# Optimization experiments

Hardware: AMD Instinct MI355X
Metric: run time of the kernel (lower is better)

The kernel has to match this reference:

```python
import jax, jax.numpy as jnp
import numpy as np

BN_EPS = 1e-5

def batchnorm2d(x, gamma, beta):
    # x: [B, H, *, *]; normalize over (B, dim2, dim3) per channel H (training-mode batch stats)
    mean = jnp.mean(x, axis=(0, 2, 3), keepdims=True)
    var = jnp.var(x, axis=(0, 2, 3), keepdims=True)
    xhat = (x - mean) * jax.lax.rsqrt(var + BN_EPS)
    return xhat * gamma[None, :, None, None] + beta[None, :, None, None]

def setup_inputs() -> dict:
    key = jax.random.key(0)
    ks = jax.random.split(key, 8)
    B, N, C = 64, 196, 768
    H = 12
    hd = C // H  # 64
    patch = 196  # img_size**2, must equal N
    x = jax.random.normal(ks[0], (B, N, C), dtype=jnp.float32)
    W_qv = jax.random.normal(ks[1], (C, 2 * C), dtype=jnp.float32) * (1.0 / np.sqrt(C))
    k_ext = jax.random.normal(ks[2], (patch, hd), dtype=jnp.float32)  # torch init: ones; randomized for testing
    attn_bias = jax.random.normal(ks[3], (1, patch), dtype=jnp.float32) * 0.02
    bn_gamma = jnp.ones((H,), dtype=jnp.float32) + 0.1 * jax.random.normal(ks[4], (H,), dtype=jnp.float32)
    bn_beta = 0.1 * jax.random.normal(ks[5], (H,), dtype=jnp.float32)
    W_proj = jax.random.normal(ks[6], (C, C), dtype=jnp.float32) * (1.0 / np.sqrt(C))
    b_proj = jnp.zeros((C,), dtype=jnp.float32)
    return {"x": x, "W_qv": W_qv, "k_ext": k_ext, "attn_bias": attn_bias,
            "bn_gamma": bn_gamma, "bn_beta": bn_beta, "W_proj": W_proj, "b_proj": b_proj}

def reference(x, W_qv, k_ext, attn_bias, bn_gamma, bn_beta, W_proj, b_proj):
    B, N, C = x.shape
    H = bn_gamma.shape[0]
    hd = C // H
    scale = hd ** -0.5
    # qv projection: [B,N,2C] -> q,v each [B,H,N,hd]
    qv = (x @ W_qv).reshape(B, N, 2, H, hd).transpose(2, 0, 3, 1, 4)
    q, v = qv[0], qv[1]
    # scores against fixed k_ext: [B,H,N,patch]
    attn = jnp.einsum('bhnd,pd->bhnp', q, k_ext)
    attn = (batchnorm2d(attn, bn_gamma, bn_beta) + attn_bias) * scale
    attn = jax.nn.softmax(attn, axis=-1)
    v = batchnorm2d(v, bn_gamma, bn_beta)
    out = jnp.einsum('bhnp,bhpd->bhnd', attn, v)  # patch == N
    out = out.transpose(0, 2, 1, 3).reshape(B, N, C)
    return out @ W_proj + b_proj
```

## Files before the change

kernel.cpp:

```cpp
#include <hip/hip_runtime.h>
#include <hip/hip_bf16.h>

typedef __bf16 b16;
typedef __bf16 b16x8 __attribute__((ext_vector_type(8)));
typedef float  f32x4 __attribute__((ext_vector_type(4)));

#define B_   64
#define N_   196
#define C_   768
#define H_   12
#define HD_  64
#define TOK  (B_*N_)
#define SCALE 0.125f

__device__ __forceinline__ void gl_lds16(const void* g, void* l){
  __builtin_amdgcn_global_load_lds((const __attribute__((address_space(1))) void*)g,
                                   (__attribute__((address_space(3))) void*)l, 16, 0, 0);
}

__global__ __launch_bounds__(256) void k_transpose_cvt(const float* __restrict__ in,
                                                       b16* __restrict__ out, int R, int C){
  __shared__ b16 tile[32][33];
  int tx = threadIdx.x, ty = threadIdx.y;
  int bx = blockIdx.x, by = blockIdx.y;
  int c = bx*32 + tx;
  #pragma unroll
  for (int i = 0; i < 32; i += 8){
    int r = by*32 + ty + i;
    tile[ty+i][tx] = (b16)in[(long)r*C + c];
  }
  __syncthreads();
  int rr = by*32 + tx;
  #pragma unroll
  for (int i = 0; i < 32; i += 8){
    int cc = bx*32 + ty + i;
    out[(long)cc*R + rr] = tile[tx][ty+i];
  }
}

__global__ __launch_bounds__(256) void k_cvt(const float* __restrict__ in, b16* __restrict__ out){
  long i = ((long)blockIdx.x*256 + threadIdx.x)*8;
  const float4* s = (const float4*)(in + i);
  float4 f0 = s[0], f1 = s[1];
  b16x8 v; v[0]=(b16)f0.x; v[1]=(b16)f0.y; v[2]=(b16)f0.z; v[3]=(b16)f0.w;
           v[4]=(b16)f1.x; v[5]=(b16)f1.y; v[6]=(b16)f1.z; v[7]=(b16)f1.w;
  *(b16x8*)(out + i) = v;
}

__global__ __launch_bounds__(256) void k_kprep(const float* __restrict__ k_ext,
                                               float* __restrict__ Kmat, float* __restrict__ ksum){
  __shared__ float ks[N_][HD_];
  int tid = threadIdx.x, blk = blockIdx.x;
  for (int i = tid; i < N_*HD_; i += 256) ks[i/HD_][i%HD_] = k_ext[i];
  __syncthreads();
  int i = tid >> 2;
  int j0 = blk*16 + (tid & 3)*4;
  float a0=0.f, a1=0.f, a2=0.f, a3=0.f;
  for (int p = 0; p < N_; ++p){
    float ki = ks[p][i];
    float4 kv = *(const float4*)&ks[p][j0];
    a0 += ki*kv.x; a1 += ki*kv.y; a2 += ki*kv.z; a3 += ki*kv.w;
  }
  Kmat[i*64+j0+0]=a0; Kmat[i*64+j0+1]=a1; Kmat[i*64+j0+2]=a2; Kmat[i*64+j0+3]=a3;
  if (blk == 0 && tid < 64){
    float s = 0.f;
    for (int p = 0; p < N_; ++p) s += ks[p][tid];
    ksum[tid] = s;
  }
}

template<int MODE>
__global__ __launch_bounds__(256) void k_gemm(const b16* __restrict__ A,
                                              const b16* __restrict__ BT,
                                              b16* __restrict__ qout, b16* __restrict__ vout,
                                              float* __restrict__ fout, const float* __restrict__ bias,
                                              const float* __restrict__ ksum, float* __restrict__ stats){
  const int NT  = (MODE == 0) ? 12 : 6;
  const int NWG = 98*NT;
  int orig = blockIdx.x;
  int q8 = NWG >> 3, r8 = NWG & 7;
  int xcd = orig & 7, loc = orig >> 3;
  int bid = (xcd < r8 ? xcd*(q8+1) : r8*(q8+1) + (xcd-r8)*q8) + loc;
  int rt = bid / NT, ct = bid % NT;
  int brow = rt*128, bcol = ct*128;

  __shared__ b16 sm[2][2][128*32];
  int tid = threadIdx.x, lane = tid & 63, w = tid >> 6;
  int wr = w >> 1, wc = w & 1;

  int rsub = w*16 + (lane>>2);
  int gsrc = (lane & 3) ^ ((lane >> 3) & 3);
  const b16* gA = A  + (long)(brow + rsub)*768 + gsrc*8;
  const b16* gB = BT + (long)(bcol + rsub)*768 + gsrc*8;
  b16* lA0 = &sm[0][0][w*16*32];
  b16* lB0 = &sm[0][1][w*16*32];
  b16* lA1 = &sm[1][0][w*16*32];
  b16* lB1 = &sm[1][1][w*16*32];

#define STAGE(la, lb, kt) do{ \
    gl_lds16(gA + (kt)*32,            (la));        \
    gl_lds16(gA + (kt)*32 + 64*768,   (la) + 64*32);\
    gl_lds16(gB + (kt)*32,            (lb));        \
    gl_lds16(gB + (kt)*32 + 64*768,   (lb) + 64*32);\
  } while(0)

#define COMPUTE(cur) do{ \
    const char* smA = (const char*)sm[cur][0]; \
    const char* smB = (const char*)sm[cur][1]; \
    b16x8 af[4], bf[4]; \
    _Pragma("unroll") \
    for (int m = 0; m < 4; ++m){ \
      int row = wr*64 + m*16 + (lane & 15); \
      af[m] = *(const b16x8*)(smA + row*64 + (((lane>>4) ^ ((row>>1)&3))<<4)); \
    } \
    _Pragma("unroll") \
    for (int n = 0; n < 4; ++n){ \
      int row = wc*64 + n*16 + (lane & 15); \
      bf[n] = *(const b16x8*)(smB + row*64 + (((lane>>4) ^ ((row>>1)&3))<<4)); \
    } \
    _Pragma("unroll") \
    for (int m = 0; m < 4; ++m) \
      _Pragma("unroll") \
      for (int n = 0; n < 4; ++n) \
        acc[m][n] = __builtin_amdgcn_mfma_f32_16x16x32_bf16(af[m], bf[n], acc[m][n], 0, 0, 0); \
  } while(0)

  f32x4 acc[4][4];
  #pragma unroll
  for (int m = 0; m < 4; ++m)
    #pragma unroll
    for (int n = 0; n < 4; ++n) acc[m][n] = (f32x4){0.f,0.f,0.f,0.f};

  STAGE(lA0, lB0, 0);
  STAGE(lA1, lB1, 1);

  #pragma unroll 1
  for (int kt = 0; kt < 23; ++kt){
    int cur = kt & 1;
    asm volatile("s_waitcnt vmcnt(4)" ::: "memory");
    __builtin_amdgcn_s_barrier();
    asm volatile("" ::: "memory");
    COMPUTE(cur);
    asm volatile("" ::: "memory");
    __builtin_amdgcn_s_barrier();
    asm volatile("" ::: "memory");
    if (kt < 22){
      if (cur == 0) STAGE(lA0, lB0, kt+2);
      else          STAGE(lA1, lB1, kt+2);
    }
  }
  asm volatile("s_waitcnt vmcnt(0)" ::: "memory");
  __builtin_amdgcn_s_barrier();
  asm volatile("" ::: "memory");
  COMPUTE(1);
#undef COMPUTE
#undef STAGE

  if constexpr (MODE == 0){
    #pragma unroll
    for (int m = 0; m < 4; ++m){
      #pragma unroll
      for (int n = 0; n < 4; ++n){
        int col = bcol + wc*64 + n*16 + (lane & 15);
        int two = (col >= 768) ? 1 : 0;
        int hc = col - two*768;
        int hh = hc >> 6, d = hc & 63;
        b16* dst = two ? vout : qout;
        #pragma unroll
        for (int j = 0; j < 4; ++j){
          int r2 = brow + wr*64 + m*16 + ((lane>>4)<<2) + j;
          int bq = r2 / 196;
          int nn = r2 - bq*196;
          dst[((bq*12 + hh)*196 + nn)*64 + d] = (b16)acc[m][n][j];
        }
      }
    }
    {
      bool isV = (bcol >= 768);
      float a_acc = 0.f, b_acc = 0.f;
      #pragma unroll
      for (int n = 0; n < 4; ++n){
        int d = n*16 + (lane & 15);
        float s = 0.f, s2 = 0.f;
        #pragma unroll
        for (int m = 0; m < 4; ++m)
          #pragma unroll
          for (int j = 0; j < 4; ++j){
            float v = acc[m][n][j];
            s += v; s2 += v*v;
          }
        if (isV){ a_acc += s; b_acc += s2; }
        else      a_acc += s * ksum[d];
      }
      #pragma unroll
      for (int off = 1; off < 64; off <<= 1){
        a_acc += __shfl_xor(a_acc, off, 64);
        b_acc += __shfl_xor(b_acc, off, 64);
      }
      if (lane == 0){
        if (isV){
          int hv = 2*(ct - 6) + wc;
          atomicAdd(&stats[24 + hv], a_acc);
          atomicAdd(&stats[36 + hv], b_acc);
        } else {
          int hq = 2*ct + wc;
          atomicAdd(&stats[hq], a_acc);
        }
      }
    }
  } else {
    #pragma unroll
    for (int m = 0; m < 4; ++m){
      #pragma unroll
      for (int n = 0; n < 4; ++n){
        int col = bcol + wc*64 + n*16 + (lane & 15);
        float bv = bias[col];
        #pragma unroll
        for (int j = 0; j < 4; ++j){
          int r2 = brow + wr*64 + m*16 + ((lane>>4)<<2) + j;
          fout[(long)r2*768 + col] = acc[m][n][j] + bv;
        }
      }
    }
  }
}

__global__ __launch_bounds__(256) void k_gram(const b16* __restrict__ qb, float* __restrict__ G){
  __shared__ b16 qT[64*232];
  int tid = threadIdx.x, lane = tid & 63, w = tid >> 6;
  int h = blockIdx.x % 12, bg = blockIdx.x / 12;
  f32x4 acc[4];
  #pragma unroll
  for (int n = 0; n < 4; ++n) acc[n] = (f32x4){0.f,0.f,0.f,0.f};
  #pragma unroll 1
  for (int r = 0; r < 2; ++r){
    int b = bg*2 + r;
    const b16* src = qb + ((long)(b*12 + h))*196*64;
    int d = lane;
    for (int p0 = w*8; p0 < 224; p0 += 32){
      b16x8 w8;
      #pragma unroll
      for (int j = 0; j < 8; ++j){
        int p = p0 + j;
        w8[j] = (p < 196) ? src[p*64 + d] : (b16)0.f;
      }
      *(b16x8*)(qT + d*232 + p0) = w8;
    }
    __syncthreads();
    #pragma unroll
    for (int ks = 0; ks < 7; ++ks){
      int t0 = ks*32;
      b16x8 af = *(const b16x8*)(qT + (16*w + (lane&15))*232 + t0 + ((lane>>4)<<3));
      #pragma unroll
      for (int n = 0; n < 4; ++n){
        b16x8 bf = *(const b16x8*)(qT + (16*n + (lane&15))*232 + t0 + ((lane>>4)<<3));
        acc[n] = __builtin_amdgcn_mfma_f32_16x16x32_bf16(af, bf, acc[n], 0, 0, 0);
      }
    }
    __syncthreads();
  }
  float* Gh = G + h*4096;
  #pragma unroll
  for (int n = 0; n < 4; ++n)
    #pragma unroll
    for (int j = 0; j < 4; ++j){
      int i  = 16*w + ((lane>>4)<<2) + j;
      int jj = 16*n + (lane&15);
      atomicAdd(&Gh[i*64 + jj], acc[n][j]);
    }
}

__global__ __launch_bounds__(256) void k_sfin(const float* __restrict__ G, const float* __restrict__ Kmat,
                                              const float* __restrict__ stats, const float* __restrict__ gamma,
                                              const float* __restrict__ beta, float* __restrict__ coef){
  int h = blockIdx.x, tid = threadIdx.x;
  const float* Gh = G + h*4096;
  float s = 0.f;
  #pragma unroll
  for (int k = 0; k < 16; ++k) s += Gh[tid + k*256]*Kmat[tid + k*256];
  #pragma unroll
  for (int off = 1; off < 64; off <<= 1) s += __shfl_xor(s, off, 64);
  __shared__ float red[4];
  if ((tid & 63) == 0) red[tid>>6] = s;
  __syncthreads();
  if (tid == 0){
    float S2 = red[0]+red[1]+red[2]+red[3];
    const float cntS = 2458624.f, cntV = 802816.f;
    float S1 = stats[h], VS = stats[24+h], VS2 = stats[36+h];
    float ms = S1/cntS;
    float vars = S2/cntS - ms*ms;
    float alpha = gamma[h]*SCALE*rsqrtf(vars + 1e-5f);
    float mv = VS/cntV;
    float varv = VS2/cntV - mv*mv;
    float a = gamma[h]*rsqrtf(varv + 1e-5f);
    coef[h*4+0] = alpha;
    coef[h*4+1] = a;
    coef[h*4+2] = beta[h] - a*mv;
  }
}

__global__ __launch_bounds__(256, 2) void k_attn(const b16* __restrict__ qb, const b16* __restrict__ vb,
                                                 const float* __restrict__ k_ext,
                                                 const float* __restrict__ attn_bias,
                                                 const float* __restrict__ coef,
                                                 b16* __restrict__ Ob){
  __shared__ b16 ksh[196*64];
  __shared__ b16 vsh[64*216];
  __shared__ b16 psh[4][16*200];
  __shared__ float bsh[196];

  int tid = threadIdx.x, lane = tid & 63, wid = tid >> 6;
  int bh = blockIdx.x;
  int h = bh % 12, b = bh / 12;
  const b16* qt = qb + (long)bh*N_*64;
  const b16* vt = vb + (long)bh*N_*64;
  float alpha = coef[h*4+0], av = coef[h*4+1], cv = coef[h*4+2];

  for (int c = tid; c < 196*8; c += 256){
    int p = c >> 3, g = c & 7;
    const float4* src = (const float4*)(k_ext + p*64 + g*8);
    float4 f0 = src[0], f1 = src[1];
    b16x8 v; v[0]=(b16)f0.x; v[1]=(b16)f0.y; v[2]=(b16)f0.z; v[3]=(b16)f0.w;
             v[4]=(b16)f1.x; v[5]=(b16)f1.y; v[6]=(b16)f1.z; v[7]=(b16)f1.w;
    *(b16x8*)((char*)ksh + p*128 + ((g ^ (p&7))<<4)) = v;
  }
  for (int p = tid; p < 196; p += 256) bsh[p] = attn_bias[p]*SCALE;
  {
    int d = tid & 63;
    for (int p0 = (tid>>6)*8; p0 < 196; p0 += 32){
      b16x8 w;
      #pragma unroll
      for (int j = 0; j < 8; ++j){
        int p = p0 + j;
        w[j] = (p < 196) ? vt[p*64 + d] : (b16)0.f;
      }
      *(b16x8*)((char*)vsh + d*432 + p0*2) = w;
    }
  }
  __syncthreads();

  for (int rt = wid; rt < 13; rt += 4){
    int n0 = rt*16;
    int qrow = n0 + (lane & 15); if (qrow > 195) qrow = 195;
    b16x8 a0 = *(const b16x8*)((const char*)qt + qrow*128 +      ((lane>>4)<<4));
    b16x8 a1 = *(const b16x8*)((const char*)qt + qrow*128 + 64 + ((lane>>4)<<4));

    f32x4 sc[13];
    #pragma unroll
    for (int ct = 0; ct < 13; ++ct){
      int p = ct*16 + (lane & 15); int pc = p > 195 ? 195 : p;
      b16x8 b0 = *(const b16x8*)((const char*)ksh + pc*128 + ((( (lane>>4))   ^ (pc&7))<<4));
      b16x8 b1 = *(const b16x8*)((const char*)ksh + pc*128 + (((4+(lane>>4))  ^ (pc&7))<<4));
      f32x4 z = {0.f,0.f,0.f,0.f};
      z = __builtin_amdgcn_mfma_f32_16x16x32_bf16(a0, b0, z, 0, 0, 0);
      z = __builtin_amdgcn_mfma_f32_16x16x32_bf16(a1, b1, z, 0, 0, 0);
      sc[ct] = z;
    }
    int pcol = lane & 15;
    float mx[4] = {-1e30f,-1e30f,-1e30f,-1e30f};
    #pragma unroll
    for (int ct = 0; ct < 13; ++ct){
      int p = ct*16 + pcol;
      bool valid = (p < 196);
      float badd = valid ? bsh[p < 196 ? p : 0] : 0.f;
      #pragma unroll
      for (int j = 0; j < 4; ++j){
        float lv = valid ? (sc[ct][j]*alpha + badd) : -1e30f;
        sc[ct][j] = lv;
        mx[j] = fmaxf(mx[j], lv);
      }
    }
    #pragma unroll
    for (int off = 1; off < 16; off <<= 1)
      #pragma unroll
      for (int j = 0; j < 4; ++j) mx[j] = fmaxf(mx[j], __shfl_xor(mx[j], off, 64));
    float sm[4] = {0.f,0.f,0.f,0.f};
    #pragma unroll
    for (int ct = 0; ct < 13; ++ct)
      #pragma unroll
      for (int j = 0; j < 4; ++j){
        float e = __expf(sc[ct][j] - mx[j]);
        sc[ct][j] = e; sm[j] += e;
      }
    #pragma unroll
    for (int off = 1; off < 16; off <<= 1)
      #pragma unroll
      for (int j = 0; j < 4; ++j) sm[j] += __shfl_xor(sm[j], off, 64);
    float rs[4];
    #pragma unroll
    for (int j = 0; j < 4; ++j) rs[j] = 1.f/sm[j];

    b16* pw = psh[wid];
    #pragma unroll
    for (int ct = 0; ct < 12; ++ct){
      int p = ct*16 + pcol;
      #pragma unroll
      for (int j = 0; j < 4; ++j){
        int r = ((lane>>4)<<2) + j;
        pw[r*200 + p] = (b16)(sc[ct][j]*rs[j]);
      }
    }
    float pt12[4];
    #pragma unroll
    for (int j = 0; j < 4; ++j) pt12[j] = sc[12][j]*rs[j];

    __asm__ volatile("s_waitcnt lgkmcnt(0)" ::: "memory");
    __builtin_amdgcn_sched_barrier(0);

    f32x4 o[4];
    #pragma unroll
    for (int dt = 0; dt < 4; ++dt) o[dt] = (f32x4){0.f,0.f,0.f,0.f};
    #pragma unroll
    for (int pt = 0; pt < 6; ++pt){
      b16x8 pa = *(const b16x8*)((const char*)pw + (lane&15)*400 + pt*64 + ((lane>>4)<<4));
      #pragma unroll
      for (int dt = 0; dt < 4; ++dt){
        b16x8 vf = *(const b16x8*)((const char*)vsh + (dt*16 + (lane&15))*432 + pt*64 + ((lane>>4)<<4));
        o[dt] = __builtin_amdgcn_mfma_f32_16x16x32_bf16(pa, vf, o[dt], 0, 0, 0);
      }
    }
    #pragma unroll
    for (int e = 0; e < 4; ++e){
      float pe[4];
      #pragma unroll
      for (int j = 0; j < 4; ++j) pe[j] = __shfl(pt12[j], (lane & 48) + e, 64);
      #pragma unroll
      for (int dt = 0; dt < 4; ++dt){
        b16 vv = *((const b16*)((const char*)vsh + (dt*16 + (lane&15))*432 + (192+e)*2));
        float vvf = (float)vv;
        #pragma unroll
        for (int j = 0; j < 4; ++j) o[dt][j] += pe[j]*vvf;
      }
    }
    #pragma unroll
    for (int dt = 0; dt < 4; ++dt)
      #pragma unroll
      for (int j = 0; j < 4; ++j){
        int n = n0 + ((lane>>4)<<2) + j;
        if (n < 196){
          long idx = ((long)(b*196 + n))*768 + h*64 + dt*16 + (lane&15);
          Ob[idx] = (b16)(av*o[dt][j] + cv);
        }
      }
  }
}

extern "C" void kernel_launch(void* const* d_in, const int* in_sizes, int n_in,
                              void* d_out, int out_size, void* d_ws, size_t ws_size,
                              hipStream_t stream){
  const float* x         = (const float*)d_in[0];
  const float* W_qv      = (const float*)d_in[1];
  const float* k_ext     = (const float*)d_in[2];
  const float* attn_bias = (const float*)d_in[3];
  const float* bn_gamma  = (const float*)d_in[4];
  const float* bn_beta   = (const float*)d_in[5];
  const float* W_proj    = (const float*)d_in[6];
  const float* b_proj    = (const float*)d_in[7];
  float* out = (float*)d_out;

  char* ws = (char*)d_ws;
  const long SZ = 19267584;
  b16*   q_buf   = (b16*)(ws);
  b16*   v_buf   = (b16*)(ws + SZ);
  b16*   O_buf   = (b16*)(ws + 2*SZ);
  b16*   x_bf16  = (b16*)(ws + 2*SZ);
  b16*   W_qvT   = (b16*)(ws + 3*SZ);
  b16*   W_projT = (b16*)(ws + 3*SZ + 2359296);
  float* Kmat    = (float*)(ws + 3*SZ + 3538944);
  float* ksum    = Kmat + 4096;
  float* stats   = ksum + 64;
  float* coef    = stats + 48;
  float* Ggram   = coef + 48;

  hipMemsetAsync(stats, 0, 48*sizeof(float), stream);
  hipMemsetAsync(Ggram, 0, 12*4096*sizeof(float), stream);

  dim3 tb(32, 8);
  k_transpose_cvt<<<dim3(1536/32, 768/32), tb, 0, stream>>>(W_qv,   W_qvT,   768, 1536);
  k_transpose_cvt<<<dim3(768/32,  768/32), tb, 0, stream>>>(W_proj, W_projT, 768, 768);
  k_cvt<<<4704, 256, 0, stream>>>(x, x_bf16);
  k_kprep<<<4, 256, 0, stream>>>(k_ext, Kmat, ksum);
  k_gemm<0><<<98*12, 256, 0, stream>>>(x_bf16, W_qvT, q_buf, v_buf, nullptr, nullptr, ksum, stats);
  k_gram<<<384, 256, 0, stream>>>(q_buf, Ggram);
  k_sfin<<<12, 256, 0, stream>>>(Ggram, Kmat, stats, bn_gamma, bn_beta, coef);
  k_attn<<<768, 256, 0, stream>>>(q_buf, v_buf, k_ext, attn_bias, coef, O_buf);
  k_gemm<1><<<98*6, 256, 0, stream>>>(O_buf, W_projT, nullptr, nullptr, out, b_proj, nullptr, nullptr);
}
```

Measured before the change: 189.2 us.

## Store q/v token-major with vectorized epilogue stores via swapped MFMA operands

The MFMA operands in the GEMM are swapped so each lane holds four consecutive output columns. This lets the epilogue write packed bf16x4 (and f32x4 with bias) vectors instead of scattered scalar stores. The q/v intermediates are now kept in token-major [B*N, 768] layout rather than head-major, and the gram and attention kernels read with a 768-element row stride. The aim is to cut store instruction count and remove the per-element div/mod index math. In exchange, the downstream per-head reads become strided.

```diff
diff --git a/kernel.cpp b/kernel.cpp
--- a/kernel.cpp
+++ b/kernel.cpp
@@ -2,6 +2,7 @@
 #include <hip/hip_bf16.h>
 
 typedef __bf16 b16;
+typedef __bf16 b16x4 __attribute__((ext_vector_type(4)));
 typedef __bf16 b16x8 __attribute__((ext_vector_type(8)));
 typedef float  f32x4 __attribute__((ext_vector_type(4)));
 
@@ -122,7 +123,7 @@
     for (int m = 0; m < 4; ++m) \
       _Pragma("unroll") \
       for (int n = 0; n < 4; ++n) \
-        acc[m][n] = __builtin_amdgcn_mfma_f32_16x16x32_bf16(af[m], bf[n], acc[m][n], 0, 0, 0); \
+        acc[m][n] = __builtin_amdgcn_mfma_f32_16x16x32_bf16(bf[n], af[m], acc[m][n], 0, 0, 0); \
   } while(0)
 
   f32x4 acc[4][4];
@@ -157,41 +158,37 @@
 #undef STAGE
 
   if constexpr (MODE == 0){
+    bool isV = (bcol >= 768);
+    b16* dst = isV ? vout : qout;
+    int cb0 = bcol - (isV ? 768 : 0) + wc*64;
     #pragma unroll
     for (int m = 0; m < 4; ++m){
+      int r2 = brow + wr*64 + m*16 + (lane & 15);
       #pragma unroll
       for (int n = 0; n < 4; ++n){
-        int col = bcol + wc*64 + n*16 + (lane & 15);
-        int two = (col >= 768) ? 1 : 0;
-        int hc = col - two*768;
-        int hh = hc >> 6, d = hc & 63;
-        b16* dst = two ? vout : qout;
+        int cc = cb0 + n*16 + ((lane>>4)<<2);
+        b16x4 pv;
+        #pragma unroll
+        for (int j = 0; j < 4; ++j) pv[j] = (b16)acc[m][n][j];
+        *(b16x4*)(dst + (long)r2*768 + cc) = pv;
+      }
+    }
+    {
+      float a_acc = 0.f, b_acc = 0.f;
+      #pragma unroll
+      for (int n = 0; n < 4; ++n)
         #pragma unroll
         for (int j = 0; j < 4; ++j){
-          int r2 = brow + wr*64 + m*16 + ((lane>>4)<<2) + j;
-          int bq = r2 / 196;
-          int nn = r2 - bq*196;
-          dst[((bq*12 + hh)*196 + nn)*64 + d] = (b16)acc[m][n][j];
-        }
-      }
-    }
-    {
-      bool isV = (bcol >= 768);
-      float a_acc = 0.f, b_acc = 0.f;
-      #pragma unroll
-      for (int n = 0; n < 4; ++n){
-        int d = n*16 + (lane & 15);
-        float s = 0.f, s2 = 0.f;
-        #pragma unroll
-        for (int m = 0; m < 4; ++m)
+          int d = n*16 + ((lane>>4)<<2) + j;
+          float s = 0.f, s2 = 0.f;
           #pragma unroll
-          for (int j = 0; j < 4; ++j){
+          for (int m = 0; m < 4; ++m){
             float v = acc[m][n][j];
             s += v; s2 += v*v;
           }
-        if (isV){ a_acc += s; b_acc += s2; }
-        else      a_acc += s * ksum[d];
-      }
+          if (isV){ a_acc += s; b_acc += s2; }
+          else      a_acc += s * ksum[d];
+        }
       #pragma unroll
       for (int off = 1; off < 64; off <<= 1){
         a_acc += __shfl_xor(a_acc, off, 64);
@@ -211,15 +208,15 @@
   } else {
     #pragma unroll
     for (int m = 0; m < 4; ++m){
+      int r2 = brow + wr*64 + m*16 + (lane & 15);
       #pragma unroll
       for (int n = 0; n < 4; ++n){
-        int col = bcol + wc*64 + n*16 + (lane & 15);
-        float bv = bias[col];
+        int cc = bcol + wc*64 + n*16 + ((lane>>4)<<2);
+        f32x4 bv = *(const f32x4*)(bias + cc);
+        f32x4 o;
         #pragma unroll
-        for (int j = 0; j < 4; ++j){
-          int r2 = brow + wr*64 + m*16 + ((lane>>4)<<2) + j;
-          fout[(long)r2*768 + col] = acc[m][n][j] + bv;
-        }
+        for (int j = 0; j < 4; ++j) o[j] = acc[m][n][j] + bv[j];
+        *(f32x4*)(fout + (long)r2*768 + cc) = o;
       }
     }
   }
@@ -235,14 +232,14 @@
   #pragma unroll 1
   for (int r = 0; r < 2; ++r){
     int b = bg*2 + r;
-    const b16* src = qb + ((long)(b*12 + h))*196*64;
+    const b16* src = qb + (long)(b*196)*768 + h*64;
     int d = lane;
     for (int p0 = w*8; p0 < 224; p0 += 32){
       b16x8 w8;
       #pragma unroll
       for (int j = 0; j < 8; ++j){
         int p = p0 + j;
-        w8[j] = (p < 196) ? src[p*64 + d] : (b16)0.f;
+        w8[j] = (p < 196) ? src[(long)p*768 + d] : (b16)0.f;
       }
       *(b16x8*)(qT + d*232 + p0) = w8;
     }
@@ -312,8 +309,8 @@
   int tid = threadIdx.x, lane = tid & 63, wid = tid >> 6;
   int bh = blockIdx.x;
   int h = bh % 12, b = bh / 12;
-  const b16* qt = qb + (long)bh*N_*64;
-  const b16* vt = vb + (long)bh*N_*64;
+  const b16* qt = qb + (long)(b*196)*768 + h*64;
+  const b16* vt = vb + (long)(b*196)*768 + h*64;
   float alpha = coef[h*4+0], av = coef[h*4+1], cv = coef[h*4+2];
 
   for (int c = tid; c < 196*8; c += 256){
@@ -332,7 +329,7 @@
       #pragma unroll
       for (int j = 0; j < 8; ++j){
         int p = p0 + j;
-        w[j] = (p < 196) ? vt[p*64 + d] : (b16)0.f;
+        w[j] = (p < 196) ? vt[(long)p*768 + d] : (b16)0.f;
       }
       *(b16x8*)((char*)vsh + d*432 + p0*2) = w;
     }
@@ -342,8 +339,8 @@
   for (int rt = wid; rt < 13; rt += 4){
     int n0 = rt*16;
     int qrow = n0 + (lane & 15); if (qrow > 195) qrow = 195;
-    b16x8 a0 = *(const b16x8*)((const char*)qt + qrow*128 +      ((lane>>4)<<4));
-    b16x8 a1 = *(const b16x8*)((const char*)qt + qrow*128 + 64 + ((lane>>4)<<4));
+    b16x8 a0 = *(const b16x8*)((const char*)qt + (long)qrow*1536 +      ((lane>>4)<<4));
+    b16x8 a1 = *(const b16x8*)((const char*)qt + (long)qrow*1536 + 64 + ((lane>>4)<<4));
 
     f32x4 sc[13];
     #pragma unroll
```

After: 196.6 us. +3.9%, slower.
